# Optimization experiments

Hardware: AMD Instinct MI355X
Metric: run time of the kernel (lower is better)

Reference implementation:

```python
import jax, jax.numpy as jnp
import numpy as np

B, T, N, D = 32, 24, 325, 64
NUM_HEADS = 8


def setup_inputs() -> dict:
    key = jax.random.key(0)
    ks = jax.random.split(key, 8)
    s = 0.02
    return {
        "X": jax.random.normal(ks[0], (B, T, N, D), dtype=jnp.float32),
        "STE": jax.random.normal(ks[1], (B, T, N, D), dtype=jnp.float32),
        "Wq": jax.random.normal(ks[2], (D, D), dtype=jnp.float32) * s,
        "bq": jnp.zeros((D,), dtype=jnp.float32),
        "Wk": jax.random.normal(ks[3], (D, D), dtype=jnp.float32) * s,
        "bk": jnp.zeros((D,), dtype=jnp.float32),
        "Wv": jax.random.normal(ks[4], (D, D), dtype=jnp.float32) * s,
        "bv": jnp.zeros((D,), dtype=jnp.float32),
        "Wf1": jax.random.normal(ks[5], (D, D), dtype=jnp.float32) * s,
        "bf1": jnp.zeros((D,), dtype=jnp.float32),
        "Wf2": jax.random.normal(ks[6], (D, D), dtype=jnp.float32) * s,
        "bf2": jnp.zeros((D,), dtype=jnp.float32),
        "K": 8,
        "d": 8,
        "bn_decay": 0,
    }


def reference(X, STE, Wq, bq, Wk, bk, Wv, bv, Wf1, bf1, Wf2, bf2, K, d, bn_decay):
    # FC projections (1x1 linear + ReLU), matching FC(emb_size, units=D, act=ReLU)
    q = jax.nn.relu(X @ Wq + bq)  # [B,T,N,D]
    k = jax.nn.relu(X @ Wk + bk)
    v = jax.nn.relu(X @ Wv + bv)
    b, t, n, dm = q.shape
    dh = dm // K  # head dim == d
    # chunk(K, dim=-1) + cat(dim=0) == split D into K heads (head k <- feature block k)
    qh = q.reshape(b, t, n, K, dh)
    kh = k.reshape(b, t, n, K, dh)
    vh = v.reshape(b, t, n, K, dh)
    # scores over temporal axis per (batch, head, node): [B,K,N,T,T]
    attn = jnp.einsum('btnkd,bsnkd->bknts', qh, kh) / jnp.sqrt(jnp.float32(d))
    # upper-triangular (incl. diagonal) kept, rest filled with -2**15 + 1
    tri = jnp.triu(jnp.ones((t, t), dtype=bool))
    attn = jnp.where(tri, attn, jnp.float32(-2 ** 15 + 1))
    attn = jax.nn.softmax(attn, axis=-1)
    out = jnp.einsum('bknts,bsnkd->btnkd', attn, vh).reshape(b, t, n, dm)
    # output FC: [D -> D (ReLU) -> D (linear)]
    h = jax.nn.relu(out @ Wf1 + bf1)
    return h @ Wf2 + bf2
```

## Files before the change

### kernel.cpp

```cpp
#include <hip/hip_runtime.h>
#include <hip/hip_bf16.h>

#define BB 32
#define TT 24
#define NN 325
#define DD 64
#define RS 68

typedef _Float16 h4 __attribute__((ext_vector_type(4)));
typedef float    f4 __attribute__((ext_vector_type(4)));

__global__ void prep_w_kernel(const float* __restrict__ Wq, const float* __restrict__ Wk,
                              const float* __restrict__ Wv, const float* __restrict__ Wf1,
                              const float* __restrict__ Wf2, _Float16* __restrict__ Wt)
{
    __shared__ float tile[64][65];
    const float* W;
    switch (blockIdx.x) {
        case 0: W = Wq; break;
        case 1: W = Wk; break;
        case 2: W = Wv; break;
        case 3: W = Wf1; break;
        default: W = Wf2; break;
    }
    const int tid = threadIdx.x;
    const int g = tid >> 6, c = tid & 63;
    #pragma unroll
    for (int p = 0; p < 16; ++p) {
        const int row = p * 4 + g;
        tile[row][c] = W[row * 64 + c];
    }
    __syncthreads();
    _Float16* dst = Wt + blockIdx.x * 4096;
    #pragma unroll
    for (int p = 0; p < 16; ++p) {
        const int col = p * 4 + g;
        dst[col * 64 + c] = (_Float16)tile[c][col];
    }
}

__global__ __launch_bounds__(256, 4) void ta_mfma_kernel(
    const float* __restrict__ X, const _Float16* __restrict__ Wt,
    const float* __restrict__ bq, const float* __restrict__ bk,
    const float* __restrict__ bv, const float* __restrict__ bf1,
    const float* __restrict__ bf2, float* __restrict__ Out)
{
    const int blk = blockIdx.x;
    const int b = blk / NN, n = blk - b * NN;
    const int tid  = threadIdx.x;
    const int lane = tid & 63;
    const int w    = tid >> 6;
    const int lr   = lane & 15;
    const int lg   = lane >> 4;

    __shared__ float qs[TT * RS];
    __shared__ float ks[TT * RS];
    __shared__ float vs[TT * RS];

    const size_t xbase = (((size_t)b * TT) * NN + n) * DD;

    h4 a[2][4];
    #pragma unroll
    for (int mt = 0; mt < 2; ++mt) {
        const int row = mt * 16 + lr;
        const bool ok = row < TT;
        const float* xp = X + xbase + (size_t)row * (NN * DD);
        #pragma unroll
        for (int kt = 0; kt < 4; ++kt) {
            f4 x = {0.f, 0.f, 0.f, 0.f};
            if (ok) x = *(const f4*)(xp + kt * 16 + lg * 4);
            h4 h;
            h[0] = (_Float16)x[0]; h[1] = (_Float16)x[1];
            h[2] = (_Float16)x[2]; h[3] = (_Float16)x[3];
            a[mt][kt] = h;
        }
    }

    const int col = 16 * w + lr;

    {
        const _Float16* wbase = Wt + col * 64 + lg * 4;
        #pragma unroll
        for (int m = 0; m < 3; ++m) {
            const float* bias = (m == 0) ? bq : (m == 1) ? bk : bv;
            float* dst        = (m == 0) ? qs : (m == 1) ? ks : vs;
            h4 bf[4];
            #pragma unroll
            for (int kt = 0; kt < 4; ++kt)
                bf[kt] = *(const h4*)(wbase + m * 4096 + kt * 16);
            const float bb = bias[col];
            f4 acc0 = {bb, bb, bb, bb};
            f4 acc1 = acc0;
            #pragma unroll
            for (int kt = 0; kt < 4; ++kt) {
                acc0 = __builtin_amdgcn_mfma_f32_16x16x16f16(a[0][kt], bf[kt], acc0, 0, 0, 0);
                acc1 = __builtin_amdgcn_mfma_f32_16x16x16f16(a[1][kt], bf[kt], acc1, 0, 0, 0);
            }
            #pragma unroll
            for (int r = 0; r < 4; ++r) {
                const int row0 = 4 * lg + r;
                dst[row0 * RS + col] = fmaxf(acc0[r], 0.f);
                const int row1 = 16 + 4 * lg + r;
                if (row1 < TT) dst[row1 * RS + col] = fmaxf(acc1[r], 0.f);
            }
        }
    }
    __syncthreads();

    if (tid < 192) {
        const int kh = tid & 7;
        const int t  = tid >> 3;
        const int t8 = w * 8;
        const int coff = kh * 8;

        const f4 qa = *(const f4*)&qs[t * RS + coff];
        const f4 qb = *(const f4*)&qs[t * RS + coff + 4];

        float sc[TT];
        float mx = -3.0e38f;
        #pragma unroll
        for (int s = 0; s < TT; ++s) {
            if (s >= t8) {
                const f4 ka = *(const f4*)&ks[s * RS + coff];
                const f4 kb = *(const f4*)&ks[s * RS + coff + 4];
                float d = qa[0]*ka[0] + qa[1]*ka[1] + qa[2]*ka[2] + qa[3]*ka[3]
                        + qb[0]*kb[0] + qb[1]*kb[1] + qb[2]*kb[2] + qb[3]*kb[3];
                d *= 0.35355339059327373f;
                d = (s >= t) ? d : -3.0e38f;
                sc[s] = d;
                mx = fmaxf(mx, d);
            }
        }
        float sum = 0.f;
        #pragma unroll
        for (int s = 0; s < TT; ++s) {
            if (s >= t8) {
                const float e = __expf(sc[s] - mx);
                sc[s] = e;
                sum += e;
            }
        }
        const float inv = 1.f / sum;
        f4 oa = {0.f, 0.f, 0.f, 0.f};
        f4 ob = {0.f, 0.f, 0.f, 0.f};
        #pragma unroll
        for (int s = 0; s < TT; ++s) {
            if (s >= t8) {
                const f4 va = *(const f4*)&vs[s * RS + coff];
                const f4 vb = *(const f4*)&vs[s * RS + coff + 4];
                const float p = sc[s];
                oa[0] += p * va[0]; oa[1] += p * va[1]; oa[2] += p * va[2]; oa[3] += p * va[3];
                ob[0] += p * vb[0]; ob[1] += p * vb[1]; ob[2] += p * vb[2]; ob[3] += p * vb[3];
            }
        }
        oa[0] *= inv; oa[1] *= inv; oa[2] *= inv; oa[3] *= inv;
        ob[0] *= inv; ob[1] *= inv; ob[2] *= inv; ob[3] *= inv;
        *(f4*)&qs[t * RS + coff]     = oa;
        *(f4*)&qs[t * RS + coff + 4] = ob;
    }
    __syncthreads();

    {
        h4 fa[2][4];
        #pragma unroll
        for (int mt = 0; mt < 2; ++mt) {
            const int row = mt * 16 + lr;
            const bool ok = row < TT;
            #pragma unroll
            for (int kt = 0; kt < 4; ++kt) {
                f4 x = {0.f, 0.f, 0.f, 0.f};
                if (ok) x = *(const f4*)&qs[row * RS + kt * 16 + lg * 4];
                h4 h;
                h[0] = (_Float16)x[0]; h[1] = (_Float16)x[1];
                h[2] = (_Float16)x[2]; h[3] = (_Float16)x[3];
                fa[mt][kt] = h;
            }
        }
        const _Float16* wp = Wt + 3 * 4096 + col * 64 + lg * 4;
        h4 bf[4];
        #pragma unroll
        for (int kt = 0; kt < 4; ++kt) bf[kt] = *(const h4*)(wp + kt * 16);
        const float bb = bf1[col];
        f4 acc0 = {bb, bb, bb, bb};
        f4 acc1 = acc0;
        #pragma unroll
        for (int kt = 0; kt < 4; ++kt) {
            acc0 = __builtin_amdgcn_mfma_f32_16x16x16f16(fa[0][kt], bf[kt], acc0, 0, 0, 0);
            acc1 = __builtin_amdgcn_mfma_f32_16x16x16f16(fa[1][kt], bf[kt], acc1, 0, 0, 0);
        }
        #pragma unroll
        for (int r = 0; r < 4; ++r) {
            const int row0 = 4 * lg + r;
            vs[row0 * RS + col] = fmaxf(acc0[r], 0.f);
            const int row1 = 16 + 4 * lg + r;
            if (row1 < TT) vs[row1 * RS + col] = fmaxf(acc1[r], 0.f);
        }
    }
    __syncthreads();

    {
        h4 fa[2][4];
        #pragma unroll
        for (int mt = 0; mt < 2; ++mt) {
            const int row = mt * 16 + lr;
            const bool ok = row < TT;
            #pragma unroll
            for (int kt = 0; kt < 4; ++kt) {
                f4 x = {0.f, 0.f, 0.f, 0.f};
                if (ok) x = *(const f4*)&vs[row * RS + kt * 16 + lg * 4];
                h4 h;
                h[0] = (_Float16)x[0]; h[1] = (_Float16)x[1];
                h[2] = (_Float16)x[2]; h[3] = (_Float16)x[3];
                fa[mt][kt] = h;
            }
        }
        const _Float16* wp = Wt + 4 * 4096 + col * 64 + lg * 4;
        h4 bf[4];
        #pragma unroll
        for (int kt = 0; kt < 4; ++kt) bf[kt] = *(const h4*)(wp + kt * 16);
        const float bb = bf2[col];
        f4 acc0 = {bb, bb, bb, bb};
        f4 acc1 = acc0;
        #pragma unroll
        for (int kt = 0; kt < 4; ++kt) {
            acc0 = __builtin_amdgcn_mfma_f32_16x16x16f16(fa[0][kt], bf[kt], acc0, 0, 0, 0);
            acc1 = __builtin_amdgcn_mfma_f32_16x16x16f16(fa[1][kt], bf[kt], acc1, 0, 0, 0);
        }
        #pragma unroll
        for (int r = 0; r < 4; ++r) {
            const int row0 = 4 * lg + r;
            Out[xbase + (size_t)row0 * (NN * DD) + col] = acc0[r];
            const int row1 = 16 + 4 * lg + r;
            if (row1 < TT) Out[xbase + (size_t)row1 * (NN * DD) + col] = acc1[r];
        }
    }
}

extern "C" void kernel_launch(void* const* d_in, const int* in_sizes, int n_in,
                              void* d_out, int out_size, void* d_ws, size_t ws_size,
                              hipStream_t stream) {
    const float* X   = (const float*)d_in[0];
    const float* Wq  = (const float*)d_in[2];
    const float* bq  = (const float*)d_in[3];
    const float* Wk  = (const float*)d_in[4];
    const float* bk  = (const float*)d_in[5];
    const float* Wv  = (const float*)d_in[6];
    const float* bv  = (const float*)d_in[7];
    const float* Wf1 = (const float*)d_in[8];
    const float* bf1 = (const float*)d_in[9];
    const float* Wf2 = (const float*)d_in[10];
    const float* bf2 = (const float*)d_in[11];
    float* Out = (float*)d_out;

    _Float16* Wt = (_Float16*)d_ws;

    prep_w_kernel<<<5, 256, 0, stream>>>(Wq, Wk, Wv, Wf1, Wf2, Wt);
    ta_mfma_kernel<<<BB * NN, 256, 0, stream>>>(X, Wt, bq, bk, bv, bf1, bf2, Out);
}
```

Measured before the change: 277.6 us.

## Process each (batch,node) in a single wavefront without block barriers, fp16 Q/K in LDS

Reassigns work so one 64-lane wavefront handles a whole (batch,node) sequence, two per 128-thread block, which removes all __syncthreads between the projection, attention and output stages. Each wave computes all four output column tiles itself. Q, K and the attention output are stored in LDS as fp16 so the next MFMA can load fragments directly, and QK dot products use packed fdot2. The costs are more serial MFMA work per wave, lower per-sequence parallelism, and extra fp16 rounding of the intermediates.

```diff
diff --git a/kernel.cpp b/kernel.cpp
--- a/kernel.cpp
+++ b/kernel.cpp
@@ -5,9 +5,11 @@
 #define TT 24
 #define NN 325
 #define DD 64
-#define RS 68
+#define RSH 72
+#define RSF 68
 
 typedef _Float16 h4 __attribute__((ext_vector_type(4)));
+typedef _Float16 h2 __attribute__((ext_vector_type(2)));
 typedef float    f4 __attribute__((ext_vector_type(4)));
 
 __global__ void prep_w_kernel(const float* __restrict__ Wq, const float* __restrict__ Wk,
@@ -39,23 +41,43 @@
     }
 }
 
-__global__ __launch_bounds__(256, 4) void ta_mfma_kernel(
+__device__ inline float dot8(h4 qa, h4 qb, h4 ka, h4 kb) {
+#if __has_builtin(__builtin_amdgcn_fdot2)
+    h2 qa0 = {qa[0], qa[1]}, qa1 = {qa[2], qa[3]};
+    h2 qb0 = {qb[0], qb[1]}, qb1 = {qb[2], qb[3]};
+    h2 ka0 = {ka[0], ka[1]}, ka1 = {ka[2], ka[3]};
+    h2 kb0 = {kb[0], kb[1]}, kb1 = {kb[2], kb[3]};
+    float d = __builtin_amdgcn_fdot2(qa0, ka0, 0.f, false);
+    d = __builtin_amdgcn_fdot2(qa1, ka1, d, false);
+    d = __builtin_amdgcn_fdot2(qb0, kb0, d, false);
+    d = __builtin_amdgcn_fdot2(qb1, kb1, d, false);
+    return d;
+#else
+    return (float)qa[0]*(float)ka[0] + (float)qa[1]*(float)ka[1]
+         + (float)qa[2]*(float)ka[2] + (float)qa[3]*(float)ka[3]
+         + (float)qb[0]*(float)kb[0] + (float)qb[1]*(float)kb[1]
+         + (float)qb[2]*(float)kb[2] + (float)qb[3]*(float)kb[3];
+#endif
+}
+
+__global__ __launch_bounds__(128) void ta_wave_kernel(
     const float* __restrict__ X, const _Float16* __restrict__ Wt,
     const float* __restrict__ bq, const float* __restrict__ bk,
     const float* __restrict__ bv, const float* __restrict__ bf1,
     const float* __restrict__ bf2, float* __restrict__ Out)
 {
-    const int blk = blockIdx.x;
-    const int b = blk / NN, n = blk - b * NN;
-    const int tid  = threadIdx.x;
-    const int lane = tid & 63;
-    const int w    = tid >> 6;
-    const int lr   = lane & 15;
-    const int lg   = lane >> 4;
-
-    __shared__ float qs[TT * RS];
-    __shared__ float ks[TT * RS];
-    __shared__ float vs[TT * RS];
+    const int wid  = threadIdx.x >> 6;
+    const int lane = threadIdx.x & 63;
+    const int gw = blockIdx.x * 2 + wid;
+    const int b = gw / NN, n = gw - b * NN;
+    const int lr = lane & 15, lg = lane >> 4;
+
+    __shared__ _Float16 qsh[2][TT * RSH];
+    __shared__ _Float16 ksh[2][TT * RSH];
+    __shared__ float    vsh[2][TT * RSF];
+    _Float16* q = qsh[wid];
+    _Float16* k = ksh[wid];
+    float*    v = vsh[wid];
 
     const size_t xbase = (((size_t)b * TT) * NN + n) * DD;
 
@@ -76,164 +98,109 @@
         }
     }
 
-    const int col = 16 * w + lr;
+#define MATMUL_NT(WOFF, BIASP, STORE)                                            \
+    {                                                                            \
+        _Pragma("unroll")                                                        \
+        for (int nt = 0; nt < 4; ++nt) {                                         \
+            const int col = 16 * nt + lr;                                        \
+            const _Float16* wp = Wt + (WOFF) + col * 64 + lg * 4;                \
+            h4 bfr[4];                                                           \
+            _Pragma("unroll")                                                    \
+            for (int kt = 0; kt < 4; ++kt) bfr[kt] = *(const h4*)(wp + kt * 16); \
+            const float bb = (BIASP)[col];                                       \
+            f4 acc0 = {bb, bb, bb, bb};                                          \
+            f4 acc1 = acc0;                                                      \
+            _Pragma("unroll")                                                    \
+            for (int kt = 0; kt < 4; ++kt) {                                     \
+                acc0 = __builtin_amdgcn_mfma_f32_16x16x16f16(a[0][kt], bfr[kt], acc0, 0, 0, 0); \
+                acc1 = __builtin_amdgcn_mfma_f32_16x16x16f16(a[1][kt], bfr[kt], acc1, 0, 0, 0); \
+            }                                                                    \
+            _Pragma("unroll")                                                    \
+            for (int r = 0; r < 4; ++r) {                                        \
+                const int row0 = 4 * lg + r;                                     \
+                const int row1 = 16 + row0;                                      \
+                STORE(row0, col, acc0[r]);                                       \
+                if (row1 < TT) STORE(row1, col, acc1[r]);                        \
+            }                                                                    \
+        }                                                                        \
+    }
+
+#define STQ(rr, cc, vv) q[(rr) * RSH + (cc)] = (_Float16)fmaxf((vv), 0.f)
+#define STK(rr, cc, vv) k[(rr) * RSH + (cc)] = (_Float16)fmaxf((vv), 0.f)
+#define STV(rr, cc, vv) v[(rr) * RSF + (cc)] = fmaxf((vv), 0.f)
+#define STH(rr, cc, vv) k[(rr) * RSH + (cc)] = (_Float16)fmaxf((vv), 0.f)
+#define STO(rr, cc, vv) Out[xbase + (size_t)(rr) * (NN * DD) + (cc)] = (vv)
+
+#define LOAD_AFRAG(SRC)                                                          \
+    {                                                                            \
+        _Pragma("unroll")                                                        \
+        for (int mt = 0; mt < 2; ++mt) {                                         \
+            const int row = 16 * mt + lr;                                        \
+            _Pragma("unroll")                                                    \
+            for (int kt = 0; kt < 4; ++kt) {                                     \
+                h4 tmpf = {(_Float16)0, (_Float16)0, (_Float16)0, (_Float16)0};  \
+                if (row < TT) tmpf = *(const h4*)&(SRC)[row * RSH + kt * 16 + lg * 4]; \
+                a[mt][kt] = tmpf;                                                \
+            }                                                                    \
+        }                                                                        \
+    }
+
+    MATMUL_NT(0 * 4096, bq, STQ)
+    MATMUL_NT(1 * 4096, bk, STK)
+    MATMUL_NT(2 * 4096, bv, STV)
 
     {
-        const _Float16* wbase = Wt + col * 64 + lg * 4;
+        const int kh = lane & 7;
+        const int tl = lane >> 3;
         #pragma unroll
-        for (int m = 0; m < 3; ++m) {
-            const float* bias = (m == 0) ? bq : (m == 1) ? bk : bv;
-            float* dst        = (m == 0) ? qs : (m == 1) ? ks : vs;
-            h4 bf[4];
-            #pragma unroll
-            for (int kt = 0; kt < 4; ++kt)
-                bf[kt] = *(const h4*)(wbase + m * 4096 + kt * 16);
-            const float bb = bias[col];
-            f4 acc0 = {bb, bb, bb, bb};
-            f4 acc1 = acc0;
-            #pragma unroll
-            for (int kt = 0; kt < 4; ++kt) {
-                acc0 = __builtin_amdgcn_mfma_f32_16x16x16f16(a[0][kt], bf[kt], acc0, 0, 0, 0);
-                acc1 = __builtin_amdgcn_mfma_f32_16x16x16f16(a[1][kt], bf[kt], acc1, 0, 0, 0);
-            }
-            #pragma unroll
-            for (int r = 0; r < 4; ++r) {
-                const int row0 = 4 * lg + r;
-                dst[row0 * RS + col] = fmaxf(acc0[r], 0.f);
-                const int row1 = 16 + 4 * lg + r;
-                if (row1 < TT) dst[row1 * RS + col] = fmaxf(acc1[r], 0.f);
-            }
-        }
-    }
-    __syncthreads();
-
-    if (tid < 192) {
-        const int kh = tid & 7;
-        const int t  = tid >> 3;
-        const int t8 = w * 8;
-        const int coff = kh * 8;
-
-        const f4 qa = *(const f4*)&qs[t * RS + coff];
-        const f4 qb = *(const f4*)&qs[t * RS + coff + 4];
-
-        float sc[TT];
-        float mx = -3.0e38f;
-        #pragma unroll
-        for (int s = 0; s < TT; ++s) {
-            if (s >= t8) {
-                const f4 ka = *(const f4*)&ks[s * RS + coff];
-                const f4 kb = *(const f4*)&ks[s * RS + coff + 4];
-                float d = qa[0]*ka[0] + qa[1]*ka[1] + qa[2]*ka[2] + qa[3]*ka[3]
-                        + qb[0]*kb[0] + qb[1]*kb[1] + qb[2]*kb[2] + qb[3]*kb[3];
-                d *= 0.35355339059327373f;
+        for (int p = 0; p < 3; ++p) {
+            const int t = 8 * p + tl;
+            const h4 qa = *(const h4*)&q[t * RSH + kh * 8];
+            const h4 qb = *(const h4*)&q[t * RSH + kh * 8 + 4];
+            float sc[TT];
+            float mx = -3.0e38f;
+            #pragma unroll
+            for (int s = 8 * p; s < TT; ++s) {
+                const h4 ka = *(const h4*)&k[s * RSH + kh * 8];
+                const h4 kb = *(const h4*)&k[s * RSH + kh * 8 + 4];
+                float d = dot8(qa, qb, ka, kb) * 0.35355339059327373f;
                 d = (s >= t) ? d : -3.0e38f;
                 sc[s] = d;
                 mx = fmaxf(mx, d);
             }
-        }
-        float sum = 0.f;
-        #pragma unroll
-        for (int s = 0; s < TT; ++s) {
-            if (s >= t8) {
+            float sum = 0.f;
+            #pragma unroll
+            for (int s = 8 * p; s < TT; ++s) {
                 const float e = __expf(sc[s] - mx);
                 sc[s] = e;
                 sum += e;
             }
+            f4 oa = {0.f, 0.f, 0.f, 0.f}, ob = {0.f, 0.f, 0.f, 0.f};
+            #pragma unroll
+            for (int s = 8 * p; s < TT; ++s) {
+                const f4 va = *(const f4*)&v[s * RSF + kh * 8];
+                const f4 vb = *(const f4*)&v[s * RSF + kh * 8 + 4];
+                const float pp = sc[s];
+                oa += pp * va;
+                ob += pp * vb;
+            }
+            const float inv = 1.f / sum;
+            h4 ha, hb;
+            #pragma unroll
+            for (int i = 0; i < 4; ++i) {
+                ha[i] = (_Float16)(oa[i] * inv);
+                hb[i] = (_Float16)(ob[i] * inv);
+            }
+            *(h4*)&q[t * RSH + kh * 8]     = ha;
+            *(h4*)&q[t * RSH + kh * 8 + 4] = hb;
         }
-        const float inv = 1.f / sum;
-        f4 oa = {0.f, 0.f, 0.f, 0.f};
-        f4 ob = {0.f, 0.f, 0.f, 0.f};
-        #pragma unroll
-        for (int s = 0; s < TT; ++s) {
-            if (s >= t8) {
-                const f4 va = *(const f4*)&vs[s * RS + coff];
-                const f4 vb = *(const f4*)&vs[s * RS + coff + 4];
-                const float p = sc[s];
-                oa[0] += p * va[0]; oa[1] += p * va[1]; oa[2] += p * va[2]; oa[3] += p * va[3];
-                ob[0] += p * vb[0]; ob[1] += p * vb[1]; ob[2] += p * vb[2]; ob[3] += p * vb[3];
-            }
-        }
-        oa[0] *= inv; oa[1] *= inv; oa[2] *= inv; oa[3] *= inv;
-        ob[0] *= inv; ob[1] *= inv; ob[2] *= inv; ob[3] *= inv;
-        *(f4*)&qs[t * RS + coff]     = oa;
-        *(f4*)&qs[t * RS + coff + 4] = ob;
-    }
-    __syncthreads();
-
-    {
-        h4 fa[2][4];
-        #pragma unroll
-        for (int mt = 0; mt < 2; ++mt) {
-            const int row = mt * 16 + lr;
-            const bool ok = row < TT;
-            #pragma unroll
-            for (int kt = 0; kt < 4; ++kt) {
-                f4 x = {0.f, 0.f, 0.f, 0.f};
-                if (ok) x = *(const f4*)&qs[row * RS + kt * 16 + lg * 4];
-                h4 h;
-                h[0] = (_Float16)x[0]; h[1] = (_Float16)x[1];
-                h[2] = (_Float16)x[2]; h[3] = (_Float16)x[3];
-                fa[mt][kt] = h;
-            }
-        }
-        const _Float16* wp = Wt + 3 * 4096 + col * 64 + lg * 4;
-        h4 bf[4];
-        #pragma unroll
-        for (int kt = 0; kt < 4; ++kt) bf[kt] = *(const h4*)(wp + kt * 16);
-        const float bb = bf1[col];
-        f4 acc0 = {bb, bb, bb, bb};
-        f4 acc1 = acc0;
-        #pragma unroll
-        for (int kt = 0; kt < 4; ++kt) {
-            acc0 = __builtin_amdgcn_mfma_f32_16x16x16f16(fa[0][kt], bf[kt], acc0, 0, 0, 0);
-            acc1 = __builtin_amdgcn_mfma_f32_16x16x16f16(fa[1][kt], bf[kt], acc1, 0, 0, 0);
-        }
-        #pragma unroll
-        for (int r = 0; r < 4; ++r) {
-            const int row0 = 4 * lg + r;
-            vs[row0 * RS + col] = fmaxf(acc0[r], 0.f);
-            const int row1 = 16 + 4 * lg + r;
-            if (row1 < TT) vs[row1 * RS + col] = fmaxf(acc1[r], 0.f);
-        }
-    }
-    __syncthreads();
-
-    {
-        h4 fa[2][4];
-        #pragma unroll
-        for (int mt = 0; mt < 2; ++mt) {
-            const int row = mt * 16 + lr;
-            const bool ok = row < TT;
-            #pragma unroll
-            for (int kt = 0; kt < 4; ++kt) {
-                f4 x = {0.f, 0.f, 0.f, 0.f};
-                if (ok) x = *(const f4*)&vs[row * RS + kt * 16 + lg * 4];
-                h4 h;
-                h[0] = (_Float16)x[0]; h[1] = (_Float16)x[1];
-                h[2] = (_Float16)x[2]; h[3] = (_Float16)x[3];
-                fa[mt][kt] = h;
-            }
-        }
-        const _Float16* wp = Wt + 4 * 4096 + col * 64 + lg * 4;
-        h4 bf[4];
-        #pragma unroll
-        for (int kt = 0; kt < 4; ++kt) bf[kt] = *(const h4*)(wp + kt * 16);
-        const float bb = bf2[col];
-        f4 acc0 = {bb, bb, bb, bb};
-        f4 acc1 = acc0;
-        #pragma unroll
-        for (int kt = 0; kt < 4; ++kt) {
-            acc0 = __builtin_amdgcn_mfma_f32_16x16x16f16(fa[0][kt], bf[kt], acc0, 0, 0, 0);
-            acc1 = __builtin_amdgcn_mfma_f32_16x16x16f16(fa[1][kt], bf[kt], acc1, 0, 0, 0);
-        }
-        #pragma unroll
-        for (int r = 0; r < 4; ++r) {
-            const int row0 = 4 * lg + r;
-            Out[xbase + (size_t)row0 * (NN * DD) + col] = acc0[r];
-            const int row1 = 16 + 4 * lg + r;
-            if (row1 < TT) Out[xbase + (size_t)row1 * (NN * DD) + col] = acc1[r];
-        }
-    }
+    }
+
+    LOAD_AFRAG(q)
+    MATMUL_NT(3 * 4096, bf1, STH)
+
+    LOAD_AFRAG(k)
+    MATMUL_NT(4 * 4096, bf2, STO)
 }
 
 extern "C" void kernel_launch(void* const* d_in, const int* in_sizes, int n_in,
@@ -255,5 +222,5 @@
     _Float16* Wt = (_Float16*)d_ws;
 
     prep_w_kernel<<<5, 256, 0, stream>>>(Wq, Wk, Wv, Wf1, Wf2, Wt);
-    ta_mfma_kernel<<<BB * NN, 256, 0, stream>>>(X, Wt, bq, bk, bv, bf1, bf2, Out);
-}
+    ta_wave_kernel<<<(BB * NN) / 2, 128, 0, stream>>>(X, Wt, bq, bk, bv, bf1, bf2, Out);
+}
```

Result: faster. 270.5 us (-2.6%).
